# Performance work log

Hardware: AMD Instinct MI355X
Metric: run time of the kernel (lower is better)

The kernel has to match this reference:

```python
import jax, jax.numpy as jnp
import numpy as np

D, VH, DFF, NL, VOCAB, NH, NKV, HD, R, SCALE = 4096, 1024, 14336, 2, 32000, 32, 8, 128, 8, 4.0
B, NIMG, T = 2, 257, 511
S = NIMG + T

def _rmsnorm(x, w, eps=1e-5):
    v = jnp.mean(jnp.square(x), axis=-1, keepdims=True)
    return x * jax.lax.rsqrt(v + eps) * w

def _lora(x, W, A, Bm):
    # base (dequantized NF4 equivalent) matmul + low-rank LoRA path, scaling = alpha/r
    base = jnp.einsum('...d,od->...o', x, W)
    low = jnp.einsum('...r,or->...o', jnp.einsum('...d,rd->...r', x, A), Bm)
    return base + low * SCALE

def _rope_tables(s):
    inv = 1.0 / (10000.0 ** (jnp.arange(0, HD, 2, dtype=jnp.float32) / HD))
    ang = jnp.arange(s, dtype=jnp.float32)[:, None] * inv[None, :]
    c, sn = jnp.cos(ang), jnp.sin(ang)
    return jnp.concatenate([c, c], -1), jnp.concatenate([sn, sn], -1)

def _apply_rope(x, cos, sin):
    rot = jnp.concatenate([-x[..., HD // 2:], x[..., :HD // 2]], -1)
    return x * cos + rot * sin

def _forward(image_embeds, proj_W, proj_b, embed, ln1, ln2, ln_f, Wq, Aq, Bq, Wk, Ak, Bk, Wv, Av, Bv, Wo, Ao, Bo, Wg, Ag, Bg, Wu, Au, Bu, Wd, Ad, Bd, input_ids, attention_mask):
    b = image_embeds.shape[0]
    img = jnp.einsum('bsv,dv->bsd', image_embeds, proj_W) + proj_b  # projector
    txt = embed[input_ids]                                          # token embedding lookup
    h = jnp.concatenate([img, txt], axis=1)                         # (B, S, D)
    s = h.shape[1]
    cos, sin = _rope_tables(s)
    allow = jnp.tril(jnp.ones((s, s), bool))[None, None] & (attention_mask[:, None, None, :] > 0)
    for i in range(NL):
        x = _rmsnorm(h, ln1[i])
        q = _lora(x, Wq[i], Aq[i], Bq[i]).reshape(b, s, NH, HD).transpose(0, 2, 1, 3)
        k = _lora(x, Wk[i], Ak[i], Bk[i]).reshape(b, s, NKV, HD).transpose(0, 2, 1, 3)
        v = _lora(x, Wv[i], Av[i], Bv[i]).reshape(b, s, NKV, HD).transpose(0, 2, 1, 3)
        q = _apply_rope(q, cos, sin)
        k = _apply_rope(k, cos, sin)
        k = jnp.repeat(k, NH // NKV, axis=1)  # GQA: expand kv heads
        v = jnp.repeat(v, NH // NKV, axis=1)
        scores = jnp.einsum('bhsd,bhtd->bhst', q, k) / jnp.sqrt(jnp.float32(HD))
        scores = jnp.where(allow, scores, jnp.float32(-1e30))
        attn = jnp.einsum('bhst,bhtd->bhsd', jax.nn.softmax(scores, axis=-1), v)
        attn = attn.transpose(0, 2, 1, 3).reshape(b, s, D)
        h = h + _lora(attn, Wo[i], Ao[i], Bo[i])
        x = _rmsnorm(h, ln2[i])
        h = h + _lora(jax.nn.silu(_lora(x, Wg[i], Ag[i], Bg[i])) * _lora(x, Wu[i], Au[i], Bu[i]), Wd[i], Ad[i], Bd[i])
    return _rmsnorm(h, ln_f)  # HF hidden_states[-1] is post final norm

def setup_inputs():
    key = jax.random.key(0)
    ks = iter(jax.random.split(key, 40))
    n = lambda shape, sc=0.02: jax.random.normal(next(ks), shape, jnp.float32) * sc
    return dict(
        image_embeds=jax.random.normal(next(ks), (B, NIMG, VH), jnp.float32),
        input_ids=jax.random.randint(next(ks), (B, T), 0, VOCAB),
        attention_mask=jnp.ones((B, S), jnp.int32),
        proj_W=n((D, VH)), proj_b=jnp.zeros((D,), jnp.float32),
        embed=n((VOCAB, D)),
        ln1=jnp.ones((NL, D), jnp.float32), ln2=jnp.ones((NL, D), jnp.float32), ln_f=jnp.ones((D,), jnp.float32),
        Wq=n((NL, D, D)), Aq=n((NL, R, D)), Bq=n((NL, D, R)),
        Wk=n((NL, NKV * HD, D)), Ak=n((NL, R, D)), Bk=n((NL, NKV * HD, R)),
        Wv=n((NL, NKV * HD, D)), Av=n((NL, R, D)), Bv=n((NL, NKV * HD, R)),
        Wo=n((NL, D, D)), Ao=n((NL, R, D)), Bo=n((NL, D, R)),
        Wg=n((NL, DFF, D)), Ag=n((NL, R, D)), Bg=n((NL, DFF, R)),
        Wu=n((NL, DFF, D)), Au=n((NL, R, D)), Bu=n((NL, DFF, R)),
        Wd=n((NL, D, DFF)), Ad=n((NL, R, DFF)), Bd=n((NL, D, R)),
    )

def reference(image_embeds, input_ids, attention_mask, proj_W, proj_b, embed, ln1, ln2, ln_f, Wq, Aq, Bq, Wk, Ak, Bk, Wv, Av, Bv, Wo, Ao, Bo, Wg, Ag, Bg, Wu, Au, Bu, Wd, Ad, Bd):
    return _forward(image_embeds, proj_W, proj_b, embed, ln1, ln2, ln_f, Wq, Aq, Bq, Wk, Ak, Bk, Wv, Av, Bv, Wo, Ao, Bo, Wg, Ag, Bg, Wu, Au, Bu, Wd, Ad, Bd, input_ids, attention_mask)
```

## Files before the change

kernel.cpp:

```cpp
#include <hip/hip_runtime.h>
#include <hip/hip_bf16.h>
#include <cstdint>
#include <cstddef>

typedef unsigned short u16;
typedef unsigned int u32;
typedef __attribute__((ext_vector_type(8))) short short8;
typedef __attribute__((ext_vector_type(4))) short short4v;
typedef __attribute__((ext_vector_type(4))) float f32x4;

__device__ __forceinline__ u16 f2bf(float f) {
  u32 u = __float_as_uint(f);
  u32 r = (u + 0x7FFFu + ((u >> 16) & 1u)) >> 16;
  return (u16)r;
}
__device__ __forceinline__ float bf2f(u16 u) {
  return __uint_as_float(((u32)u) << 16);
}
__device__ __forceinline__ short f2bf_hw(float f) {
  union { __hip_bfloat16 h; u16 u; } c;
  c.h = __float2bfloat16(f);
  return (short)c.u;
}

__device__ __forceinline__ void gload_lds16(const void* g, void* l) {
  __builtin_amdgcn_global_load_lds((const __attribute__((address_space(1))) void*)g,
                                   (__attribute__((address_space(3))) void*)l, 16, 0, 0);
}

struct GemmArgs {
  const u16* A; int M; int K; int lda;
  const float* W0; const float* LB0; int toff0;
  const float* W1; const float* LB1; int toff1;
  const float* W2; const float* LB2; int toff2;
  int ldw;
  int seg1; int seg2;
  const float* t;
  const float* bias;
  const float* resid;
  float* outf; int ostride;
  u16* outb0; u16* outb1;
  int rowremap;
  float* outp;
};

__global__ __launch_bounds__(256) void gemm_kernel(GemmArgs a) {
  __shared__ u16   Asm[128 * 64];
  __shared__ float BsmF[128 * 64];
  const int tid = threadIdx.x;

  const int nwg = gridDim.x * gridDim.y;
  const int bid0 = blockIdx.y * gridDim.x + blockIdx.x;
  const int q = nwg >> 3, r = nwg & 7;
  const int xcd = bid0 & 7, pos = bid0 >> 3;
  const int nb = (xcd < r ? xcd * (q + 1) : r * (q + 1) + (xcd - r) * q) + pos;
  const int m0 = (nb % gridDim.x) * 128;
  const int n0 = (nb / gridDim.x) * 128;

  const float* W = a.W0; const float* LB = a.LB0; int toff = a.toff0; int nbase = 0;
  if (a.seg2 && n0 >= a.seg2)      { W = a.W2; LB = a.LB2; toff = a.toff2; nbase = a.seg2; }
  else if (a.seg1 && n0 >= a.seg1) { W = a.W1; LB = a.LB1; toff = a.toff1; nbase = a.seg1; }
  const int koff = blockIdx.z * a.K;
  const u16* Ab = a.A + koff;
  const float* Wt = W + (size_t)(n0 - nbase) * a.ldw + koff;

  const int lane = tid & 63, wid = tid >> 6;
  const int wr = wid >> 1, wcn = wid & 1;
  const int lrow = lane & 15, g = lane >> 4;
  const int arow = lane >> 3;
  const int aslot = (lane & 7) ^ arow;
  const int brow4 = lane >> 4;

  f32x4 acc[4][4] = {};

  auto dma_A = [&](int k0) {
#pragma unroll
    for (int i = 0; i < 4; i++) {
      int c = wid * 4 + i;
      const u16* src = Ab + (size_t)(m0 + c * 8 + arow) * a.lda + k0 + (aslot << 3);
      gload_lds16(src, &Asm[c * 512]);
    }
  };
  auto dma_B = [&](int k0) {
#pragma unroll
    for (int j = 0; j < 8; j++) {
      int rrow = wid * 32 + j * 4 + brow4;
      int sslot = (lane & 15) ^ (rrow & 7);
      const float* src = Wt + (size_t)rrow * a.ldw + k0 + (sslot << 2);
      gload_lds16(src, &BsmF[(wid * 32 + j * 4) * 64]);
    }
  };

  dma_A(0);
  dma_B(0);
  const int nk = a.K >> 6;
  for (int kt = 0; kt < nk; kt++) {
    __syncthreads();

    short8 af[4][2], bq[4][2];
#pragma unroll
    for (int mi = 0; mi < 4; mi++) {
      int row = wr * 64 + mi * 16 + lrow;
#pragma unroll
      for (int x = 0; x < 2; x++) {
        int s = x * 4 + g;
        af[mi][x] = *(const short8*)&Asm[row * 64 + ((s ^ (lrow & 7)) << 3)];
      }
    }
#pragma unroll
    for (int ni = 0; ni < 4; ni++) {
      int row = wcn * 64 + ni * 16 + lrow;
      int m = row & 7;
      const float* bp = &BsmF[row * 64];
#pragma unroll
      for (int x = 0; x < 2; x++) {
        int sg0 = x * 8 + g * 2;
        f32x4 lo = *(const f32x4*)(bp + ((sg0 ^ m) << 2));
        f32x4 hi = *(const f32x4*)(bp + (((sg0 + 1) ^ m) << 2));
        short8 sv;
        sv[0] = f2bf_hw(lo[0]); sv[1] = f2bf_hw(lo[1]);
        sv[2] = f2bf_hw(lo[2]); sv[3] = f2bf_hw(lo[3]);
        sv[4] = f2bf_hw(hi[0]); sv[5] = f2bf_hw(hi[1]);
        sv[6] = f2bf_hw(hi[2]); sv[7] = f2bf_hw(hi[3]);
        bq[ni][x] = sv;
      }
    }

    asm volatile("s_waitcnt lgkmcnt(0)" ::: "memory");
    __builtin_amdgcn_sched_barrier(0);
    __builtin_amdgcn_s_barrier();
    __builtin_amdgcn_sched_barrier(0);
    if (kt + 1 < nk) {
      dma_A((kt + 1) << 6);
      dma_B((kt + 1) << 6);
    }
#pragma unroll
    for (int x = 0; x < 2; x++)
#pragma unroll
      for (int mi = 0; mi < 4; mi++)
#pragma unroll
        for (int ni = 0; ni < 4; ni++)
          acc[mi][ni] = __builtin_amdgcn_mfma_f32_16x16x32_bf16(af[mi][x], bq[ni][x], acc[mi][ni], 0, 0, 0);
  }

  if (a.outp) {
    float* op = a.outp + (size_t)blockIdx.z * (1536 * 4096);
#pragma unroll
    for (int mi = 0; mi < 4; mi++)
#pragma unroll
      for (int rr = 0; rr < 4; rr++) {
        int row = m0 + wr * 64 + mi * 16 + (g << 2) + rr;
#pragma unroll
        for (int ni = 0; ni < 4; ni++) {
          int n = n0 + wcn * 64 + ni * 16 + lrow;
          op[(size_t)row * a.ostride + n] = acc[mi][ni][rr];
        }
      }
    return;
  }
  const bool dolora = (a.t != nullptr);
  float lbv[4][8];
#pragma unroll
  for (int ni = 0; ni < 4; ni++) {
    if (dolora) {
      int cl = wcn * 64 + ni * 16 + lrow;
      const float* bp = LB + (size_t)(n0 - nbase + cl) * 8;
#pragma unroll
      for (int r2 = 0; r2 < 8; r2++) lbv[ni][r2] = bp[r2];
    }
  }
#pragma unroll
  for (int mi = 0; mi < 4; mi++) {
#pragma unroll
    for (int rr = 0; rr < 4; rr++) {
      int row = m0 + wr * 64 + mi * 16 + (g << 2) + rr;
      if (row >= a.M) continue;
      float tv[8];
      if (dolora) {
        const float* tp = a.t + row * 32 + toff;
#pragma unroll
        for (int r2 = 0; r2 < 8; r2++) tv[r2] = tp[r2];
      }
#pragma unroll
      for (int ni = 0; ni < 4; ni++) {
        int n = n0 + wcn * 64 + ni * 16 + lrow;
        float val = acc[mi][ni][rr];
        if (dolora) {
          float ds = 0.f;
#pragma unroll
          for (int r2 = 0; r2 < 8; r2++) ds += tv[r2] * lbv[ni][r2];
          val += 4.0f * ds;
        }
        if (a.bias)  val += a.bias[n];
        if (a.resid) val += a.resid[(size_t)row * 4096 + n];
        if (a.outf) {
          int orow = a.rowremap ? (row < 257 ? row : row + 511) : row;
          a.outf[(size_t)orow * a.ostride + n] = val;
        } else if (a.seg1 && n >= a.seg1) {
          a.outb1[(size_t)row * a.ostride + (n - a.seg1)] = f2bf(val);
        } else {
          a.outb0[(size_t)row * a.ostride + n] = f2bf(val);
        }
      }
    }
  }
}

__global__ __launch_bounds__(256) void combine_kernel(float* __restrict__ h,
    const float* __restrict__ p, const float* __restrict__ t,
    const float* __restrict__ LB) {
  const int row = blockIdx.x;
  float tv[8];
  const float* tp = t + row * 32;
#pragma unroll
  for (int r = 0; r < 8; r++) tv[r] = tp[r];
  const float* p1 = p + (size_t)1536 * 4096;
#pragma unroll
  for (int i = 0; i < 4; i++) {
    int base = threadIdx.x * 4 + i * 1024;
    size_t off = (size_t)row * 4096 + base;
    float4 hv = *(const float4*)(h + off);
    float4 a0 = *(const float4*)(p + off);
    float4 a1 = *(const float4*)(p1 + off);
    float o[4] = {hv.x + a0.x + a1.x, hv.y + a0.y + a1.y,
                  hv.z + a0.z + a1.z, hv.w + a0.w + a1.w};
#pragma unroll
    for (int j = 0; j < 4; j++) {
      const float* lb = LB + (size_t)(base + j) * 8;
      float ds = 0.f;
#pragma unroll
      for (int r = 0; r < 8; r++) ds += tv[r] * lb[r];
      o[j] += 4.0f * ds;
    }
    float4 ov; ov.x = o[0]; ov.y = o[1]; ov.z = o[2]; ov.w = o[3];
    *(float4*)(h + off) = ov;
  }
}

template<int NA>
__global__ __launch_bounds__(256) void lora_xa_kernel(const u16* __restrict__ X, int K,
    const float* A0, const float* A1, const float* A2, float* __restrict__ t) {
  const int m = blockIdx.x;
  const u16* xr = X + (size_t)m * K;
  float acc[NA * 8];
#pragma unroll
  for (int i = 0; i < NA * 8; i++) acc[i] = 0.f;
  const float* Ap[3] = {A0, A1, A2};
  for (int k = threadIdx.x * 8; k < K; k += 2048) {
    uint4 xv = *(const uint4*)(xr + k);
    float xf[8];
    xf[0] = bf2f((u16)(xv.x & 0xffff)); xf[1] = bf2f((u16)(xv.x >> 16));
    xf[2] = bf2f((u16)(xv.y & 0xffff)); xf[3] = bf2f((u16)(xv.y >> 16));
    xf[4] = bf2f((u16)(xv.z & 0xffff)); xf[5] = bf2f((u16)(xv.z >> 16));
    xf[6] = bf2f((u16)(xv.w & 0xffff)); xf[7] = bf2f((u16)(xv.w >> 16));
#pragma unroll
    for (int aa = 0; aa < NA; aa++) {
#pragma unroll
      for (int r = 0; r < 8; r++) {
        const float* ar = Ap[aa] + (size_t)r * K + k;
        float4 a0 = *(const float4*)ar;
        float4 a1 = *(const float4*)(ar + 4);
        acc[aa * 8 + r] += xf[0] * a0.x + xf[1] * a0.y + xf[2] * a0.z + xf[3] * a0.w
                         + xf[4] * a1.x + xf[5] * a1.y + xf[6] * a1.z + xf[7] * a1.w;
      }
    }
  }
  __shared__ float red[4][NA * 8];
#pragma unroll
  for (int i = 0; i < NA * 8; i++) {
    float v = acc[i];
#pragma unroll
    for (int o = 1; o < 64; o <<= 1) v += __shfl_xor(v, o);
    if ((threadIdx.x & 63) == 0) red[threadIdx.x >> 6][i] = v;
  }
  __syncthreads();
  if (threadIdx.x < NA * 8)
    t[m * 32 + threadIdx.x] = red[0][threadIdx.x] + red[1][threadIdx.x]
                            + red[2][threadIdx.x] + red[3][threadIdx.x];
}

__global__ __launch_bounds__(256) void rmsnorm_kernel(const float* __restrict__ h,
    const float* __restrict__ w, u16* outb, float* outf) {
  const int m = blockIdx.x;
  const float* row = h + (size_t)m * 4096;
  float4 v[4];
  float ss = 0.f;
#pragma unroll
  for (int i = 0; i < 4; i++) {
    v[i] = *(const float4*)(row + threadIdx.x * 4 + i * 1024);
    ss += v[i].x * v[i].x + v[i].y * v[i].y + v[i].z * v[i].z + v[i].w * v[i].w;
  }
#pragma unroll
  for (int o = 1; o < 64; o <<= 1) ss += __shfl_xor(ss, o);
  __shared__ float red[4];
  if ((threadIdx.x & 63) == 0) red[threadIdx.x >> 6] = ss;
  __syncthreads();
  ss = red[0] + red[1] + red[2] + red[3];
  float rs = rsqrtf(ss * (1.f / 4096.f) + 1e-5f);
#pragma unroll
  for (int i = 0; i < 4; i++) {
    int base = threadIdx.x * 4 + i * 1024;
    float4 wv = *(const float4*)(w + base);
    float o0 = v[i].x * rs * wv.x, o1 = v[i].y * rs * wv.y;
    float o2 = v[i].z * rs * wv.z, o3 = v[i].w * rs * wv.w;
    if (outb) {
      short4v sv; sv.x = (short)f2bf(o0); sv.y = (short)f2bf(o1);
      sv.z = (short)f2bf(o2); sv.w = (short)f2bf(o3);
      *(short4v*)(outb + (size_t)m * 4096 + base) = sv;
    } else {
      float4 ov; ov.x = o0; ov.y = o1; ov.z = o2; ov.w = o3;
      *(float4*)(outf + (size_t)m * 4096 + base) = ov;
    }
  }
}

__global__ void rope_tab_kernel(float2* __restrict__ tab) {
  int idx = blockIdx.x * 256 + threadIdx.x;
  int s = idx >> 6, i = idx & 63;
  float inv = __expf(-(float)i * (9.210340371976184f / 64.f));
  float ang = (float)s * inv;
  float sn, cs;
  sincosf(ang, &sn, &cs);
  float2 r; r.x = cs; r.y = sn;
  tab[idx] = r;
}

__global__ __launch_bounds__(256) void rope_apply_kernel(float* __restrict__ qkv,
    const float2* __restrict__ tab) {
  int m = blockIdx.x;
  int s = m % 768;
  float* rowp = qkv + (size_t)m * 6144;
  for (int idx = threadIdx.x; idx < 2560; idx += 256) {
    int head = idx >> 6, i = idx & 63;
    int col = (head < 32) ? head * 128 : 4096 + (head - 32) * 128;
    float2 cs = tab[s * 64 + i];
    float x0 = rowp[col + i], x1 = rowp[col + i + 64];
    rowp[col + i]      = x0 * cs.x - x1 * cs.y;
    rowp[col + i + 64] = x1 * cs.x + x0 * cs.y;
  }
}

__global__ __launch_bounds__(256) void attn_mfma_kernel(const float* __restrict__ qkv,
    const int* __restrict__ amask, u16* __restrict__ attn_bf) {
  __shared__ u16 Ks[4][32][40];
  __shared__ u16 Vt[128][40];
  __shared__ u16 Ps[4][16][40];
  const int b = blockIdx.z, hh = blockIdx.y, q0 = blockIdx.x * 64;
  const int kvh = hh >> 2;
  const int tid = threadIdx.x, lane = tid & 63, w = tid >> 6;
  const int lrow = lane & 15, g = lane >> 4;
  const float sc = 0.08838834764831845f;

  short8 qf[4];
  {
    const float* qp = qkv + ((size_t)(b * 768 + q0 + w * 16 + lrow)) * 6144 + hh * 128;
#pragma unroll
    for (int ks = 0; ks < 4; ks++) {
      float4 lo = *(const float4*)(qp + ks * 32 + g * 8);
      float4 hi = *(const float4*)(qp + ks * 32 + g * 8 + 4);
      short8 sv;
      sv[0] = f2bf_hw(lo.x * sc); sv[1] = f2bf_hw(lo.y * sc);
      sv[2] = f2bf_hw(lo.z * sc); sv[3] = f2bf_hw(lo.w * sc);
      sv[4] = f2bf_hw(hi.x * sc); sv[5] = f2bf_hw(hi.y * sc);
      sv[6] = f2bf_hw(hi.z * sc); sv[7] = f2bf_hw(hi.w * sc);
      qf[ks] = sv;
    }
  }

  f32x4 acco[8] = {};
  float mrun[4] = {-1e30f, -1e30f, -1e30f, -1e30f};
  float lrun[4] = {0.f, 0.f, 0.f, 0.f};
  const int ntile = (q0 >> 5) + 2;

  for (int kt = 0; kt < ntile; kt++) {
    const int k0 = kt * 32;
    __syncthreads();
#pragma unroll
    for (int i = 0; i < 4; i++) {
      int idx = i * 256 + tid;
      int r2 = idx >> 5, c4 = (idx & 31) << 2;
      const float* kp = qkv + ((size_t)(b * 768 + k0 + r2)) * 6144 + 4096 + kvh * 128 + c4;
      float4 kv = *(const float4*)kp;
      short4v ksv;
      ksv.x = f2bf_hw(kv.x); ksv.y = f2bf_hw(kv.y);
      ksv.z = f2bf_hw(kv.z); ksv.w = f2bf_hw(kv.w);
      *(short4v*)&Ks[c4 >> 5][r2][c4 & 31] = ksv;
      float4 vv = *(const float4*)(kp + 1024);
      Vt[c4 + 0][r2] = (u16)f2bf_hw(vv.x);
      Vt[c4 + 1][r2] = (u16)f2bf_hw(vv.y);
      Vt[c4 + 2][r2] = (u16)f2bf_hw(vv.z);
      Vt[c4 + 3][r2] = (u16)f2bf_hw(vv.w);
    }
    __syncthreads();

    f32x4 s0 = {}, s1 = {};
#pragma unroll
    for (int ks = 0; ks < 4; ks++) {
      short8 kb0 = *(const short8*)&Ks[ks][lrow][g * 8];
      short8 kb1 = *(const short8*)&Ks[ks][16 + lrow][g * 8];
      s0 = __builtin_amdgcn_mfma_f32_16x16x32_bf16(qf[ks], kb0, s0, 0, 0, 0);
      s1 = __builtin_amdgcn_mfma_f32_16x16x32_bf16(qf[ks], kb1, s1, 0, 0, 0);
    }
    const int key0 = k0 + lrow, key1 = k0 + 16 + lrow;
    const bool am0 = amask[b * 768 + key0] != 0;
    const bool am1 = amask[b * 768 + key1] != 0;
    float scl4[4];
#pragma unroll
    for (int rr = 0; rr < 4; rr++) {
      int qrow = q0 + w * 16 + g * 4 + rr;
      float v0 = (key0 <= qrow && am0) ? s0[rr] : -1e30f;
      float v1 = (key1 <= qrow && am1) ? s1[rr] : -1e30f;
      float m = fmaxf(v0, v1);
      m = fmaxf(m, __shfl_xor(m, 1));
      m = fmaxf(m, __shfl_xor(m, 2));
      m = fmaxf(m, __shfl_xor(m, 4));
      m = fmaxf(m, __shfl_xor(m, 8));
      float mnew = fmaxf(mrun[rr], m);
      float scl = __expf(mrun[rr] - mnew);
      float p0 = __expf(v0 - mnew);
      float p1 = __expf(v1 - mnew);
      float ls = p0 + p1;
      ls += __shfl_xor(ls, 1);
      ls += __shfl_xor(ls, 2);
      ls += __shfl_xor(ls, 4);
      ls += __shfl_xor(ls, 8);
      lrun[rr] = lrun[rr] * scl + ls;
      mrun[rr] = mnew;
      scl4[rr] = scl;
      Ps[w][g * 4 + rr][lrow]      = (u16)f2bf_hw(p0);
      Ps[w][g * 4 + rr][16 + lrow] = (u16)f2bf_hw(p1);
    }
#pragma unroll
    for (int nf = 0; nf < 8; nf++)
#pragma unroll
      for (int rr = 0; rr < 4; rr++) acco[nf][rr] *= scl4[rr];

    asm volatile("s_waitcnt lgkmcnt(0)" ::: "memory");
    __builtin_amdgcn_sched_barrier(0);
    short8 pa = *(const short8*)&Ps[w][lrow][g * 8];
#pragma unroll
    for (int nf = 0; nf < 8; nf++) {
      short8 vb = *(const short8*)&Vt[nf * 16 + lrow][g * 8];
      acco[nf] = __builtin_amdgcn_mfma_f32_16x16x32_bf16(pa, vb, acco[nf], 0, 0, 0);
    }
  }

#pragma unroll
  for (int rr = 0; rr < 4; rr++) {
    float inv = 1.f / lrun[rr];
    size_t orow = (size_t)(b * 768 + q0 + w * 16 + g * 4 + rr);
#pragma unroll
    for (int nf = 0; nf < 8; nf++)
      attn_bf[orow * 4096 + hh * 128 + nf * 16 + lrow] = f2bf(acco[nf][rr] * inv);
  }
}

__global__ void convert_img_kernel(const float* __restrict__ in, u16* __restrict__ out) {
  int idx = blockIdx.x * 256 + threadIdx.x;
  if (idx >= 81920) return;
  uint4 w = {0u, 0u, 0u, 0u};
  if (idx < 65792) {
    const float* p = in + (size_t)idx * 8;
    float4 v0 = *(const float4*)p;
    float4 v1 = *(const float4*)(p + 4);
    w.x = (u32)f2bf(v0.x) | ((u32)f2bf(v0.y) << 16);
    w.y = (u32)f2bf(v0.z) | ((u32)f2bf(v0.w) << 16);
    w.z = (u32)f2bf(v1.x) | ((u32)f2bf(v1.y) << 16);
    w.w = (u32)f2bf(v1.z) | ((u32)f2bf(v1.w) << 16);
  }
  *(uint4*)(out + (size_t)idx * 8) = w;
}

__global__ void embed_gather_kernel(const float* __restrict__ embed,
    const int* __restrict__ ids, float* __restrict__ h) {
  int row = blockIdx.x;
  int b = row / 511, tt = row % 511;
  int id = ids[b * 511 + tt];
  const float* src = embed + (size_t)id * 4096;
  float* dst = h + ((size_t)(b * 768 + 257 + tt)) * 4096;
  for (int i = threadIdx.x * 4; i < 4096; i += 1024)
    *(float4*)(dst + i) = *(const float4*)(src + i);
}

__global__ __launch_bounds__(256) void gu_combine_kernel(const u16* __restrict__ g,
    const u16* __restrict__ u, u16* __restrict__ x2) {
  size_t idx = (size_t)blockIdx.x * 256 + threadIdx.x;
  uint4 gv = *(const uint4*)(g + idx * 8);
  uint4 uv = *(const uint4*)(u + idx * 8);
  u32 gi[4] = {gv.x, gv.y, gv.z, gv.w};
  u32 ui[4] = {uv.x, uv.y, uv.z, uv.w};
  u32 oi[4];
#pragma unroll
  for (int i = 0; i < 4; i++) {
    float g0 = bf2f((u16)(gi[i] & 0xffff)), g1 = bf2f((u16)(gi[i] >> 16));
    float u0 = bf2f((u16)(ui[i] & 0xffff)), u1 = bf2f((u16)(ui[i] >> 16));
    float s0 = g0 / (1.f + __expf(-g0)) * u0;
    float s1 = g1 / (1.f + __expf(-g1)) * u1;
    oi[i] = (u32)f2bf(s0) | ((u32)f2bf(s1) << 16);
  }
  uint4 ov; ov.x = oi[0]; ov.y = oi[1]; ov.z = oi[2]; ov.w = oi[3];
  *(uint4*)(x2 + idx * 8) = ov;
}

extern "C" void kernel_launch(void* const* d_in, const int* in_sizes, int n_in,
                              void* d_out, int out_size, void* d_ws, size_t ws_size,
                              hipStream_t stream) {
  const float* image_embeds = (const float*)d_in[0];
  const int*   input_ids    = (const int*)d_in[1];
  const int*   amask        = (const int*)d_in[2];
  const float* proj_W = (const float*)d_in[3];
  const float* proj_b = (const float*)d_in[4];
  const float* embed  = (const float*)d_in[5];
  const float* ln1 = (const float*)d_in[6];
  const float* ln2 = (const float*)d_in[7];
  const float* ln_f = (const float*)d_in[8];
  const float* Wq = (const float*)d_in[9];
  const float* Aq = (const float*)d_in[10];
  const float* Bq = (const float*)d_in[11];
  const float* Wk = (const float*)d_in[12];
  const float* Ak = (const float*)d_in[13];
  const float* Bk = (const float*)d_in[14];
  const float* Wv = (const float*)d_in[15];
  const float* Av = (const float*)d_in[16];
  const float* Bv = (const float*)d_in[17];
  const float* Wo = (const float*)d_in[18];
  const float* Ao = (const float*)d_in[19];
  const float* Bo = (const float*)d_in[20];
  const float* Wg = (const float*)d_in[21];
  const float* Ag = (const float*)d_in[22];
  const float* Bg = (const float*)d_in[23];
  const float* Wu = (const float*)d_in[24];
  const float* Au = (const float*)d_in[25];
  const float* Bu = (const float*)d_in[26];
  const float* Wd = (const float*)d_in[27];
  const float* Ad = (const float*)d_in[28];
  const float* Bd = (const float*)d_in[29];
  (void)in_sizes; (void)n_in; (void)out_size; (void)ws_size;

  char* ws = (char*)d_ws;
  size_t off = 0;
  auto alloc = [&](size_t bytes) -> void* {
    void* p = ws + off; off += (bytes + 255) & ~(size_t)255; return p;
  };
  float* h       = (float*) alloc((size_t)1536 * 4096 * 4);
  u16*   xn      = (u16*)   alloc((size_t)1536 * 4096 * 2);
  float* qkv     = (float*) alloc((size_t)1536 * 6144 * 4);
  u16*   attn_bf = (u16*)   alloc((size_t)1536 * 4096 * 2);
  u16*   g_bf    = (u16*)   alloc((size_t)1536 * 14336 * 2);
  u16*   u_bf    = (u16*)   alloc((size_t)1536 * 14336 * 2);
  u16*   x2_bf   = (u16*)   alloc((size_t)1536 * 14336 * 2);
  float* t       = (float*) alloc((size_t)1536 * 32 * 4);
  float2* tab    = (float2*)alloc((size_t)768 * 64 * 8);
  u16*   img_bf  = (u16*)   alloc((size_t)640 * 1024 * 2);
  float* pc      = (float*) alloc((size_t)2 * 1536 * 4096 * 4);

  dim3 blk(256);
  convert_img_kernel<<<dim3(320), blk, 0, stream>>>(image_embeds, img_bf);
  rope_tab_kernel<<<dim3(192), blk, 0, stream>>>(tab);

  {
    GemmArgs a = {};
    a.A = img_bf; a.M = 514; a.K = 1024; a.lda = 1024; a.ldw = 1024;
    a.W0 = proj_W;
    a.bias = proj_b;
    a.outf = h; a.ostride = 4096; a.rowremap = 1;
    gemm_kernel<<<dim3(5, 32), blk, 0, stream>>>(a);
  }
  embed_gather_kernel<<<dim3(1022), blk, 0, stream>>>(embed, input_ids, h);

  for (int l = 0; l < 2; l++) {
    const float* Wq_l = Wq + (size_t)l * 4096 * 4096;
    const float* Aq_l = Aq + (size_t)l * 8 * 4096;
    const float* Bq_l = Bq + (size_t)l * 4096 * 8;
    const float* Wk_l = Wk + (size_t)l * 1024 * 4096;
    const float* Ak_l = Ak + (size_t)l * 8 * 4096;
    const float* Bk_l = Bk + (size_t)l * 1024 * 8;
    const float* Wv_l = Wv + (size_t)l * 1024 * 4096;
    const float* Av_l = Av + (size_t)l * 8 * 4096;
    const float* Bv_l = Bv + (size_t)l * 1024 * 8;
    const float* Wo_l = Wo + (size_t)l * 4096 * 4096;
    const float* Ao_l = Ao + (size_t)l * 8 * 4096;
    const float* Bo_l = Bo + (size_t)l * 4096 * 8;
    const float* Wg_l = Wg + (size_t)l * 14336 * 4096;
    const float* Ag_l = Ag + (size_t)l * 8 * 4096;
    const float* Bg_l = Bg + (size_t)l * 14336 * 8;
    const float* Wu_l = Wu + (size_t)l * 14336 * 4096;
    const float* Au_l = Au + (size_t)l * 8 * 4096;
    const float* Bu_l = Bu + (size_t)l * 14336 * 8;
    const float* Wd_l = Wd + (size_t)l * 4096 * 14336;
    const float* Ad_l = Ad + (size_t)l * 8 * 14336;
    const float* Bd_l = Bd + (size_t)l * 4096 * 8;

    rmsnorm_kernel<<<dim3(1536), blk, 0, stream>>>(h, ln1 + l * 4096, xn, (float*)nullptr);
    lora_xa_kernel<3><<<dim3(1536), blk, 0, stream>>>(xn, 4096, Aq_l, Ak_l, Av_l, t);
    {
      GemmArgs a = {};
      a.A = xn; a.M = 1536; a.K = 4096; a.lda = 4096; a.ldw = 4096;
      a.W0 = Wq_l; a.LB0 = Bq_l; a.toff0 = 0;
      a.W1 = Wk_l; a.LB1 = Bk_l; a.toff1 = 8;
      a.W2 = Wv_l; a.LB2 = Bv_l; a.toff2 = 16;
      a.seg1 = 4096; a.seg2 = 5120;
      a.t = t; a.outf = qkv; a.ostride = 6144;
      gemm_kernel<<<dim3(12, 48), blk, 0, stream>>>(a);
    }
    rope_apply_kernel<<<dim3(1536), blk, 0, stream>>>(qkv, tab);
    attn_mfma_kernel<<<dim3(12, 32, 2), blk, 0, stream>>>(qkv, amask, attn_bf);
    lora_xa_kernel<1><<<dim3(1536), blk, 0, stream>>>(attn_bf, 4096, Ao_l,
        (const float*)nullptr, (const float*)nullptr, t);
    {
      GemmArgs a = {};
      a.A = attn_bf; a.M = 1536; a.K = 2048; a.lda = 4096; a.ldw = 4096;
      a.W0 = Wo_l;
      a.ostride = 4096; a.outp = pc;
      gemm_kernel<<<dim3(12, 32, 2), blk, 0, stream>>>(a);
      combine_kernel<<<dim3(1536), blk, 0, stream>>>(h, pc, t, Bo_l);
    }
    rmsnorm_kernel<<<dim3(1536), blk, 0, stream>>>(h, ln2 + l * 4096, xn, (float*)nullptr);
    lora_xa_kernel<2><<<dim3(1536), blk, 0, stream>>>(xn, 4096, Ag_l, Au_l,
        (const float*)nullptr, t);
    {
      GemmArgs a = {};
      a.A = xn; a.M = 1536; a.K = 4096; a.lda = 4096; a.ldw = 4096;
      a.W0 = Wg_l; a.LB0 = Bg_l; a.toff0 = 0;
      a.W1 = Wu_l; a.LB1 = Bu_l; a.toff1 = 8;
      a.seg1 = 14336;
      a.t = t; a.outb0 = g_bf; a.outb1 = u_bf; a.ostride = 14336;
      gemm_kernel<<<dim3(12, 224), blk, 0, stream>>>(a);
    }
    gu_combine_kernel<<<dim3(10752), blk, 0, stream>>>(g_bf, u_bf, x2_bf);
    lora_xa_kernel<1><<<dim3(1536), blk, 0, stream>>>(x2_bf, 14336, Ad_l,
        (const float*)nullptr, (const float*)nullptr, t);
    {
      GemmArgs a = {};
      a.A = x2_bf; a.M = 1536; a.K = 7168; a.lda = 14336; a.ldw = 14336;
      a.W0 = Wd_l;
      a.ostride = 4096; a.outp = pc;
      gemm_kernel<<<dim3(12, 32, 2), blk, 0, stream>>>(a);
      combine_kernel<<<dim3(1536), blk, 0, stream>>>(h, pc, t, Bd_l);
    }
  }
  rmsnorm_kernel<<<dim3(1536), blk, 0, stream>>>(h, ln_f, (u16*)nullptr, (float*)d_out);
}
```

Before: 3.210 ms.

## Pre-convert fp32 weights to bf16 in workspace before GEMMs

Adds a kernel that converts all layer weight matrices from fp32 to bf16 into the workspace at the start of each call. The GEMM kernel gains a bf16-weight mode that DMAs half-size B tiles into LDS and skips the per-tile float-to-bf16 conversion. This trades an extra full pass over the weights (read fp32, write bf16) for lower weight bandwidth and less ALU work inside the GEMMs. It falls back to the old path if the workspace is too small.

```diff
diff --git a/kernel.cpp b/kernel.cpp
--- a/kernel.cpp
+++ b/kernel.cpp
@@ -28,11 +28,28 @@
                                    (__attribute__((address_space(3))) void*)l, 16, 0, 0);
 }
 
+__global__ __launch_bounds__(256) void convert_w_kernel(const float* __restrict__ src,
+    u16* __restrict__ dst, long n8) {
+  long stride = (long)gridDim.x * 256;
+  for (long i = (long)blockIdx.x * 256 + threadIdx.x; i < n8; i += stride) {
+    const float* p = src + i * 8;
+    float4 v0 = *(const float4*)p;
+    float4 v1 = *(const float4*)(p + 4);
+    uint4 w;
+    w.x = (u32)(u16)f2bf_hw(v0.x) | ((u32)(u16)f2bf_hw(v0.y) << 16);
+    w.y = (u32)(u16)f2bf_hw(v0.z) | ((u32)(u16)f2bf_hw(v0.w) << 16);
+    w.z = (u32)(u16)f2bf_hw(v1.x) | ((u32)(u16)f2bf_hw(v1.y) << 16);
+    w.w = (u32)(u16)f2bf_hw(v1.z) | ((u32)(u16)f2bf_hw(v1.w) << 16);
+    *(uint4*)(dst + i * 8) = w;
+  }
+}
+
 struct GemmArgs {
   const u16* A; int M; int K; int lda;
   const float* W0; const float* LB0; int toff0;
   const float* W1; const float* LB1; int toff1;
   const float* W2; const float* LB2; int toff2;
+  const u16* Wb0; const u16* Wb1; const u16* Wb2;
   int ldw;
   int seg1; int seg2;
   const float* t;
@@ -44,9 +61,10 @@
   float* outp;
 };
 
+template<int WMODE>
 __global__ __launch_bounds__(256) void gemm_kernel(GemmArgs a) {
-  __shared__ u16   Asm[128 * 64];
-  __shared__ float BsmF[128 * 64];
+  __shared__ u16 Asm[128 * 64];
+  __shared__ u16 BsmW[WMODE ? 128 * 64 : 128 * 128];
   const int tid = threadIdx.x;
 
   const int nwg = gridDim.x * gridDim.y;
@@ -57,12 +75,14 @@
   const int m0 = (nb % gridDim.x) * 128;
   const int n0 = (nb / gridDim.x) * 128;
 
-  const float* W = a.W0; const float* LB = a.LB0; int toff = a.toff0; int nbase = 0;
-  if (a.seg2 && n0 >= a.seg2)      { W = a.W2; LB = a.LB2; toff = a.toff2; nbase = a.seg2; }
-  else if (a.seg1 && n0 >= a.seg1) { W = a.W1; LB = a.LB1; toff = a.toff1; nbase = a.seg1; }
+  const float* W = a.W0; const u16* Wb = a.Wb0;
+  const float* LB = a.LB0; int toff = a.toff0; int nbase = 0;
+  if (a.seg2 && n0 >= a.seg2)      { W = a.W2; Wb = a.Wb2; LB = a.LB2; toff = a.toff2; nbase = a.seg2; }
+  else if (a.seg1 && n0 >= a.seg1) { W = a.W1; Wb = a.Wb1; LB = a.LB1; toff = a.toff1; nbase = a.seg1; }
   const int koff = blockIdx.z * a.K;
   const u16* Ab = a.A + koff;
   const float* Wt = W + (size_t)(n0 - nbase) * a.ldw + koff;
+  const u16* Wbt = Wb + (size_t)(n0 - nbase) * a.ldw + koff;
 
   const int lane = tid & 63, wid = tid >> 6;
   const int wr = wid >> 1, wcn = wid & 1;
@@ -82,12 +102,22 @@
     }
   };
   auto dma_B = [&](int k0) {
-#pragma unroll
-    for (int j = 0; j < 8; j++) {
-      int rrow = wid * 32 + j * 4 + brow4;
-      int sslot = (lane & 15) ^ (rrow & 7);
-      const float* src = Wt + (size_t)rrow * a.ldw + k0 + (sslot << 2);
-      gload_lds16(src, &BsmF[(wid * 32 + j * 4) * 64]);
+    if (WMODE) {
+#pragma unroll
+      for (int i = 0; i < 4; i++) {
+        int c = wid * 4 + i;
+        const u16* src = Wbt + (size_t)(c * 8 + arow) * a.ldw + k0 + (aslot << 3);
+        gload_lds16(src, &BsmW[c * 512]);
+      }
+    } else {
+      float* Bf = (float*)BsmW;
+#pragma unroll
+      for (int j = 0; j < 8; j++) {
+        int rrow = wid * 32 + j * 4 + brow4;
+        int sslot = (lane & 15) ^ (rrow & 7);
+        const float* src = Wt + (size_t)rrow * a.ldw + k0 + (sslot << 2);
+        gload_lds16(src, &Bf[(wid * 32 + j * 4) * 64]);
+      }
     }
   };
 
@@ -110,19 +140,27 @@
 #pragma unroll
     for (int ni = 0; ni < 4; ni++) {
       int row = wcn * 64 + ni * 16 + lrow;
-      int m = row & 7;
-      const float* bp = &BsmF[row * 64];
-#pragma unroll
-      for (int x = 0; x < 2; x++) {
-        int sg0 = x * 8 + g * 2;
-        f32x4 lo = *(const f32x4*)(bp + ((sg0 ^ m) << 2));
-        f32x4 hi = *(const f32x4*)(bp + (((sg0 + 1) ^ m) << 2));
-        short8 sv;
-        sv[0] = f2bf_hw(lo[0]); sv[1] = f2bf_hw(lo[1]);
-        sv[2] = f2bf_hw(lo[2]); sv[3] = f2bf_hw(lo[3]);
-        sv[4] = f2bf_hw(hi[0]); sv[5] = f2bf_hw(hi[1]);
-        sv[6] = f2bf_hw(hi[2]); sv[7] = f2bf_hw(hi[3]);
-        bq[ni][x] = sv;
+      if (WMODE) {
+#pragma unroll
+        for (int x = 0; x < 2; x++) {
+          int s = x * 4 + g;
+          bq[ni][x] = *(const short8*)&BsmW[row * 64 + ((s ^ (lrow & 7)) << 3)];
+        }
+      } else {
+        const float* bp = (const float*)BsmW + row * 64;
+        int m = row & 7;
+#pragma unroll
+        for (int x = 0; x < 2; x++) {
+          int sg0 = x * 8 + g * 2;
+          f32x4 lo = *(const f32x4*)(bp + ((sg0 ^ m) << 2));
+          f32x4 hi = *(const f32x4*)(bp + (((sg0 + 1) ^ m) << 2));
+          short8 sv;
+          sv[0] = f2bf_hw(lo[0]); sv[1] = f2bf_hw(lo[1]);
+          sv[2] = f2bf_hw(lo[2]); sv[3] = f2bf_hw(lo[3]);
+          sv[4] = f2bf_hw(hi[0]); sv[5] = f2bf_hw(hi[1]);
+          sv[6] = f2bf_hw(hi[2]); sv[7] = f2bf_hw(hi[3]);
+          bq[ni][x] = sv;
+        }
       }
     }
 
@@ -535,7 +573,7 @@
   const float* Wd = (const float*)d_in[27];
   const float* Ad = (const float*)d_in[28];
   const float* Bd = (const float*)d_in[29];
-  (void)in_sizes; (void)n_in; (void)out_size; (void)ws_size;
+  (void)in_sizes; (void)n_in; (void)out_size;
 
   char* ws = (char*)d_ws;
   size_t off = 0;
@@ -553,8 +591,33 @@
   float2* tab    = (float2*)alloc((size_t)768 * 64 * 8);
   u16*   img_bf  = (u16*)   alloc((size_t)640 * 1024 * 2);
   float* pc      = (float*) alloc((size_t)2 * 1536 * 4096 * 4);
+  const size_t nQ = (size_t)2 * 4096 * 4096;
+  const size_t nK = (size_t)2 * 1024 * 4096;
+  const size_t nG = (size_t)2 * 14336 * 4096;
+  u16* wq_b = (u16*)alloc(nQ * 2);
+  u16* wk_b = (u16*)alloc(nK * 2);
+  u16* wv_b = (u16*)alloc(nK * 2);
+  u16* wo_b = (u16*)alloc(nQ * 2);
+  u16* wg_b = (u16*)alloc(nG * 2);
+  u16* wu_b = (u16*)alloc(nG * 2);
+  u16* wd_b = (u16*)alloc(nG * 2);
+  const bool use_bf = (off <= ws_size);
 
   dim3 blk(256);
+  if (use_bf) {
+    convert_w_kernel<<<dim3(2048), blk, 0, stream>>>(Wq, wq_b, (long)(nQ / 8));
+    convert_w_kernel<<<dim3(1024), blk, 0, stream>>>(Wk, wk_b, (long)(nK / 8));
+    convert_w_kernel<<<dim3(1024), blk, 0, stream>>>(Wv, wv_b, (long)(nK / 8));
+    convert_w_kernel<<<dim3(2048), blk, 0, stream>>>(Wo, wo_b, (long)(nQ / 8));
+    convert_w_kernel<<<dim3(2048), blk, 0, stream>>>(Wg, wg_b, (long)(nG / 8));
+    convert_w_kernel<<<dim3(2048), blk, 0, stream>>>(Wu, wu_b, (long)(nG / 8));
+    convert_w_kernel<<<dim3(2048), blk, 0, stream>>>(Wd, wd_b, (long)(nG / 8));
+  }
+  auto launch_gemm = [&](const GemmArgs& a, dim3 grid) {
+    if (a.Wb0) gemm_kernel<1><<<grid, blk, 0, stream>>>(a);
+    else       gemm_kernel<0><<<grid, blk, 0, stream>>>(a);
+  };
+
   convert_img_kernel<<<dim3(320), blk, 0, stream>>>(image_embeds, img_bf);
   rope_tab_kernel<<<dim3(192), blk, 0, stream>>>(tab);
 
@@ -564,7 +627,7 @@
     a.W0 = proj_W;
     a.bias = proj_b;
     a.outf = h; a.ostride = 4096; a.rowremap = 1;
-    gemm_kernel<<<dim3(5, 32), blk, 0, stream>>>(a);
+    launch_gemm(a, dim3(5, 32));
   }
   embed_gather_kernel<<<dim3(1022), blk, 0, stream>>>(embed, input_ids, h);
 
@@ -590,6 +653,13 @@
     const float* Wd_l = Wd + (size_t)l * 4096 * 14336;
     const float* Ad_l = Ad + (size_t)l * 8 * 14336;
     const float* Bd_l = Bd + (size_t)l * 4096 * 8;
+    const u16* wq_bl = use_bf ? wq_b + (size_t)l * 4096 * 4096 : nullptr;
+    const u16* wk_bl = use_bf ? wk_b + (size_t)l * 1024 * 4096 : nullptr;
+    const u16* wv_bl = use_bf ? wv_b + (size_t)l * 1024 * 4096 : nullptr;
+    const u16* wo_bl = use_bf ? wo_b + (size_t)l * 4096 * 4096 : nullptr;
+    const u16* wg_bl = use_bf ? wg_b + (size_t)l * 14336 * 4096 : nullptr;
+    const u16* wu_bl = use_bf ? wu_b + (size_t)l * 14336 * 4096 : nullptr;
+    const u16* wd_bl = use_bf ? wd_b + (size_t)l * 14336 * 4096 : nullptr;
 
     rmsnorm_kernel<<<dim3(1536), blk, 0, stream>>>(h, ln1 + l * 4096, xn, (float*)nullptr);
     lora_xa_kernel<3><<<dim3(1536), blk, 0, stream>>>(xn, 4096, Aq_l, Ak_l, Av_l, t);
@@ -599,9 +669,10 @@
       a.W0 = Wq_l; a.LB0 = Bq_l; a.toff0 = 0;
       a.W1 = Wk_l; a.LB1 = Bk_l; a.toff1 = 8;
       a.W2 = Wv_l; a.LB2 = Bv_l; a.toff2 = 16;
+      a.Wb0 = wq_bl; a.Wb1 = wk_bl; a.Wb2 = wv_bl;
       a.seg1 = 4096; a.seg2 = 5120;
       a.t = t; a.outf = qkv; a.ostride = 6144;
-      gemm_kernel<<<dim3(12, 48), blk, 0, stream>>>(a);
+      launch_gemm(a, dim3(12, 48));
     }
     rope_apply_kernel<<<dim3(1536), blk, 0, stream>>>(qkv, tab);
     attn_mfma_kernel<<<dim3(12, 32, 2), blk, 0, stream>>>(qkv, amask, attn_bf);
@@ -610,9 +681,9 @@
     {
       GemmArgs a = {};
       a.A = attn_bf; a.M = 1536; a.K = 2048; a.lda = 4096; a.ldw = 4096;
-      a.W0 = Wo_l;
+      a.W0 = Wo_l; a.Wb0 = wo_bl;
       a.ostride = 4096; a.outp = pc;
-      gemm_kernel<<<dim3(12, 32, 2), blk, 0, stream>>>(a);
+      launch_gemm(a, dim3(12, 32, 2));
       combine_kernel<<<dim3(1536), blk, 0, stream>>>(h, pc, t, Bo_l);
     }
     rmsnorm_kernel<<<dim3(1536), blk, 0, stream>>>(h, ln2 + l * 4096, xn, (float*)nullptr);
@@ -623,9 +694,10 @@
       a.A = xn; a.M = 1536; a.K = 4096; a.lda = 4096; a.ldw = 4096;
       a.W0 = Wg_l; a.LB0 = Bg_l; a.toff0 = 0;
       a.W1 = Wu_l; a.LB1 = Bu_l; a.toff1 = 8;
+      a.Wb0 = wg_bl; a.Wb1 = wu_bl;
       a.seg1 = 14336;
       a.t = t; a.outb0 = g_bf; a.outb1 = u_bf; a.ostride = 14336;
-      gemm_kernel<<<dim3(12, 224), blk, 0, stream>>>(a);
+      launch_gemm(a, dim3(12, 224));
     }
     gu_combine_kernel<<<dim3(10752), blk, 0, stream>>>(g_bf, u_bf, x2_bf);
     lora_xa_kernel<1><<<dim3(1536), blk, 0, stream>>>(x2_bf, 14336, Ad_l,
@@ -633,9 +705,9 @@
     {
       GemmArgs a = {};
       a.A = x2_bf; a.M = 1536; a.K = 7168; a.lda = 14336; a.ldw = 14336;
-      a.W0 = Wd_l;
+      a.W0 = Wd_l; a.Wb0 = wd_bl;
       a.ostride = 4096; a.outp = pc;
-      gemm_kernel<<<dim3(12, 32, 2), blk, 0, stream>>>(a);
+      launch_gemm(a, dim3(12, 32, 2));
       combine_kernel<<<dim3(1536), blk, 0, stream>>>(h, pc, t, Bd_l);
     }
   }
```

New measurement: 3.185 ms. Within noise of the previous version (-0.8%).
